# Kernel optimization log

Measured on AMD Instinct MI355X. Metric: run time of the kernel, lower is better.

## Reference

```python
import jax, jax.numpy as jnp
import numpy as np

DIM = 768
HEADS = 12
HEAD_DIM = DIM // HEADS


def setup_inputs() -> dict:
    key = jax.random.key(0)
    ks = jax.random.split(key, 5)
    B, N = 2, 2048
    x = jax.random.normal(ks[0], (B, N, DIM), dtype=jnp.float32)
    s = 1.0 / np.sqrt(DIM)
    qkv_w = jax.random.normal(ks[1], (3 * DIM, DIM), dtype=jnp.float32) * s
    qkv_b = jnp.zeros((3 * DIM,), dtype=jnp.float32)
    proj_w = jax.random.normal(ks[2], (DIM, DIM), dtype=jnp.float32) * s
    proj_b = jnp.zeros((DIM,), dtype=jnp.float32)
    return {"x": x, "qkv_w": qkv_w, "qkv_b": qkv_b, "proj_w": proj_w, "proj_b": proj_b}


def reference(x, qkv_w, qkv_b, proj_w, proj_b):
    B, N, C = x.shape
    scale = HEAD_DIM ** -0.5
    qkv = x @ qkv_w.T + qkv_b                      # [B,N,3C]
    qkv = qkv.reshape(B, N, 3, HEADS, HEAD_DIM)
    q = qkv[:, :, 0].transpose(0, 2, 1, 3)         # [B,H,N,D]
    k = qkv[:, :, 1].transpose(0, 2, 1, 3)
    v = qkv[:, :, 2].transpose(0, 2, 1, 3)
    attn = jnp.einsum('bhnd,bhmd->bhnm', q, k) * scale
    attn = jax.nn.softmax(attn, axis=-1)
    out = jnp.einsum('bhnm,bhmd->bhnd', attn, v)   # [B,H,N,D]
    out = out.transpose(0, 2, 1, 3).reshape(B, N, C)
    return out @ proj_w.T + proj_b
```

## Files before the change

kernel.cpp:

```cpp
#include <hip/hip_runtime.h>
#include <hip/hip_bf16.h>

typedef __bf16 bf16x8 __attribute__((ext_vector_type(8)));
typedef float f32x4 __attribute__((ext_vector_type(4)));
typedef float f32x16 __attribute__((ext_vector_type(16)));

#define SEQ   2048
#define NHEAD 12
#define NBH   24
#define QSCALE 0.18033688011112042f

#define CP16(g, l) __builtin_amdgcn_global_load_lds( \
    (const __attribute__((address_space(1))) unsigned int*)(g), \
    (__attribute__((address_space(3))) unsigned int*)(l), 16, 0, 0)

#define SUPER 1040
__device__ __forceinline__ int ldsoffK(int R, int c) {
  return (R >> 3) * SUPER + (R & 7) * 128 + ((c ^ (R & 7)) << 4);
}

__device__ __forceinline__ unsigned short f2bf(float f) {
  unsigned int u = __builtin_bit_cast(unsigned int, f);
  u += 0x7FFFu + ((u >> 16) & 1u);
  return (unsigned short)(u >> 16);
}
__device__ __forceinline__ unsigned int packbf2_trunc(float lo, float hi) {
  return __builtin_amdgcn_perm(__builtin_bit_cast(unsigned int, hi),
                               __builtin_bit_cast(unsigned int, lo), 0x07060302u);
}

#define NX4  786432
#define NW14 442368
__global__ __launch_bounds__(256) void cvt3_kernel(const float4* __restrict__ x,
                                                   const float4* __restrict__ w1,
                                                   const float4* __restrict__ w2,
                                                   ushort4* __restrict__ xo,
                                                   ushort4* __restrict__ w1o,
                                                   ushort4* __restrict__ w2o) {
  int i = blockIdx.x * 256 + threadIdx.x;
  const float4* s;
  ushort4* d;
  int j = i;
  if (i < NX4)               { s = x;  d = xo; }
  else if (i < NX4 + NW14)   { s = w1; d = w1o; j = i - NX4; }
  else                       { s = w2; d = w2o; j = i - (NX4 + NW14); }
  float4 v = s[j];
  ushort4 r;
  r.x = f2bf(v.x); r.y = f2bf(v.y); r.z = f2bf(v.z); r.w = f2bf(v.w);
  d[j] = r;
}

template <int BM, int BN, int MODE>
__global__ __launch_bounds__(256) void gemm_kernel(const unsigned short* __restrict__ X,
                                                   const unsigned short* __restrict__ W,
                                                   const float* __restrict__ bias,
                                                   unsigned short* __restrict__ Qb,
                                                   unsigned short* __restrict__ Kb,
                                                   unsigned short* __restrict__ Vtb,
                                                   float* __restrict__ Out) {
  constexpr int K = 768, BK = 64;
  constexpr int WM = BM / 2, WN = BN / 2;
  constexpr int MT = WM / 16, NT = WN / 16;
  __shared__ __align__(16) char Xs[(BM / 8) * SUPER];
  __shared__ __align__(16) char Ws[(BN / 8) * SUPER];

  const int tid = threadIdx.x;
  const int w = tid >> 6, lane = tid & 63, quad = lane >> 4, m16 = lane & 15;
  const int wm = w & 1, wn = w >> 1;
  const int row0 = blockIdx.y * BM, col0 = blockIdx.x * BN;

  f32x4 acc[MT][NT];
#pragma unroll
  for (int mt = 0; mt < MT; ++mt)
#pragma unroll
    for (int nt = 0; nt < NT; ++nt) acc[mt][nt] = (f32x4){0.f, 0.f, 0.f, 0.f};

  for (int k0 = 0; k0 < K; k0 += BK) {
    __syncthreads();
#pragma unroll
    for (int j = 0; j < BM / 32; ++j) {
      int e = tid + 256 * j, r = e >> 3, c8 = e & 7;
      CP16(X + (size_t)(row0 + r) * 768 + k0 + ((c8 ^ (r & 7)) << 3),
           Xs + (w + 4 * j) * SUPER + lane * 16);
    }
#pragma unroll
    for (int j = 0; j < BN / 32; ++j) {
      int e = tid + 256 * j, r = e >> 3, c8 = e & 7;
      CP16(W + (size_t)(col0 + r) * 768 + k0 + ((c8 ^ (r & 7)) << 3),
           Ws + (w + 4 * j) * SUPER + lane * 16);
    }
    __syncthreads();
#pragma unroll
    for (int ks = 0; ks < 2; ++ks) {
      bf16x8 a[MT], b[NT];
#pragma unroll
      for (int mt = 0; mt < MT; ++mt)
        a[mt] = *(const bf16x8*)(Xs + ldsoffK(wm * WM + mt * 16 + m16, quad + 4 * ks));
#pragma unroll
      for (int nt = 0; nt < NT; ++nt)
        b[nt] = *(const bf16x8*)(Ws + ldsoffK(wn * WN + nt * 16 + m16, quad + 4 * ks));
#pragma unroll
      for (int mt = 0; mt < MT; ++mt)
#pragma unroll
        for (int nt = 0; nt < NT; ++nt)
          acc[mt][nt] = __builtin_amdgcn_mfma_f32_16x16x32_bf16(a[mt], b[nt], acc[mt][nt], 0, 0, 0);
    }
  }

#pragma unroll
  for (int mt = 0; mt < MT; ++mt) {
#pragma unroll
    for (int nt = 0; nt < NT; ++nt) {
      const int m0 = row0 + wm * WM + mt * 16 + quad * 4;
      const int c = col0 + wn * WN + nt * 16 + m16;
      const float bia = bias[c];
      f32x4 v = acc[mt][nt];
      if constexpr (MODE == 0) {
        const int bidx = m0 >> 11, ns = m0 & 2047;
        if (c < 1536) {
          unsigned short* dst;
          float sc;
          int cc;
          if (c < 768) { cc = c; dst = Qb; sc = QSCALE; }
          else         { cc = c - 768; dst = Kb; sc = 1.0f; }
          const int h = cc >> 6, d = cc & 63;
          unsigned short* p = dst + ((size_t)(bidx * NHEAD + h) * SEQ + ns) * 64 + d;
          p[0]   = f2bf((v[0] + bia) * sc);
          p[64]  = f2bf((v[1] + bia) * sc);
          p[128] = f2bf((v[2] + bia) * sc);
          p[192] = f2bf((v[3] + bia) * sc);
        } else {
          const int cc = c - 1536, h = cc >> 6, d = cc & 63;
          const int ns2 = (ns & ~12) | ((ns & 4) << 1) | ((ns & 8) >> 1);
          ushort4 pk;
          pk.x = f2bf(v[0] + bia); pk.y = f2bf(v[1] + bia);
          pk.z = f2bf(v[2] + bia); pk.w = f2bf(v[3] + bia);
          *(ushort4*)(Vtb + ((size_t)(bidx * NHEAD + h) * 64 + d) * SEQ + ns2) = pk;
        }
      } else {
        float* o = Out + (size_t)m0 * 768 + c;
        o[0]       = v[0] + bia;
        o[768]     = v[1] + bia;
        o[2 * 768] = v[2] + bia;
        o[3 * 768] = v[3] + bia;
      }
    }
  }
}

__global__ __launch_bounds__(256, 3) void attn_kernel(const unsigned short* __restrict__ Qb,
                                                      const unsigned short* __restrict__ Kb,
                                                      const unsigned short* __restrict__ Vtb,
                                                      unsigned short* __restrict__ Ab) {
  __shared__ __align__(16) char KsB[2][2][4 * SUPER];
  __shared__ __align__(16) float Comb[2][2][4][64][4];
  __shared__ float Lc[2][64];

  const int tid = threadIdx.x;
  const int w = tid >> 6, lane = tid & 63, hi = lane >> 5, l32 = lane & 31;
  const int pair = w >> 1, qtile = w & 1;
  const int bh = blockIdx.x % NBH, qt = blockIdx.x / NBH;
  const int bb = bh / NHEAD, h = bh % NHEAD;
  const int q0 = qt * 64 + qtile * 32;

  const unsigned short* Qp = Qb + (size_t)bh * SEQ * 64;
  const unsigned short* Kph = Kb + (size_t)bh * SEQ * 64 + (size_t)pair * 1024 * 64;
  const unsigned short* vp0 = Vtb + (size_t)bh * 64 * SEQ + (size_t)l32 * SEQ + pair * 1024 + hi * 8;
  const unsigned short* vp1 = vp0 + (size_t)32 * SEQ;

  bf16x8 qf[4];
#pragma unroll
  for (int dc = 0; dc < 4; ++dc)
    qf[dc] = *(const bf16x8*)(Qp + (size_t)(q0 + l32) * 64 + dc * 16 + hi * 8);

  const unsigned short* srcK[2];
  int dK[2];
#pragma unroll
  for (int jj = 0; jj < 2; ++jj) {
    int e = qtile * 128 + jj * 64 + lane, r = e >> 3, c8 = e & 7;
    srcK[jj] = Kph + r * 64 + ((c8 ^ (r & 7)) << 3);
    dK[jj] = (qtile * 2 + jj) * SUPER + lane * 16;
  }
  int koff[4];
#pragma unroll
  for (int dc = 0; dc < 4; ++dc) koff[dc] = ldsoffK(l32, (dc << 1) | hi);

#pragma unroll
  for (int jj = 0; jj < 2; ++jj) CP16(srcK[jj], &KsB[pair][0][dK[jj]]);
  bf16x8 vfA[4], vfB[4];
  vfA[0] = *(const bf16x8*)(vp0);
  vfA[1] = *(const bf16x8*)(vp0 + 16);
  vfA[2] = *(const bf16x8*)(vp1);
  vfA[3] = *(const bf16x8*)(vp1 + 16);

  f32x16 o[2] = {};
  float l_i = 0.f;

#define ATTN_STEP(BUF, VC, VN, IT)                                                  \
  {                                                                                 \
    __syncthreads();                                                                \
    const char* kb = KsB[pair][BUF];                                                \
    bf16x8 kf[4];                                                                   \
    _Pragma("unroll") for (int dc = 0; dc < 4; ++dc)                                \
      kf[dc] = *(const bf16x8*)(kb + koff[dc]);                                     \
    if ((IT) < 31) {                                                                \
      _Pragma("unroll") for (int jj = 0; jj < 2; ++jj) {                            \
        srcK[jj] += 2048;                                                           \
        CP16(srcK[jj], &KsB[pair][1 - (BUF)][dK[jj]]);                              \
      }                                                                             \
      vp0 += 32; vp1 += 32;                                                         \
      VN[0] = *(const bf16x8*)(vp0);                                                \
      VN[1] = *(const bf16x8*)(vp0 + 16);                                           \
      VN[2] = *(const bf16x8*)(vp1);                                                \
      VN[3] = *(const bf16x8*)(vp1 + 16);                                           \
    }                                                                               \
    f32x16 s = {};                                                                  \
    _Pragma("unroll") for (int dc = 0; dc < 4; ++dc)                                \
      s = __builtin_amdgcn_mfma_f32_32x32x16_bf16(kf[dc], qf[dc], s, 0, 0, 0);      \
    float pv[16];                                                                   \
    _Pragma("unroll") for (int e = 0; e < 16; ++e)                                  \
      pv[e] = __builtin_amdgcn_exp2f(s[e]);                                         \
    float t0 = (pv[0] + pv[1]) + (pv[2] + pv[3]);                                   \
    float t1 = (pv[4] + pv[5]) + (pv[6] + pv[7]);                                   \
    float t2 = (pv[8] + pv[9]) + (pv[10] + pv[11]);                                 \
    float t3 = (pv[12] + pv[13]) + (pv[14] + pv[15]);                               \
    l_i += (t0 + t1) + (t2 + t3);                                                   \
    unsigned int pf[8];                                                             \
    _Pragma("unroll") for (int e2 = 0; e2 < 8; ++e2)                                \
      pf[e2] = packbf2_trunc(pv[2 * e2], pv[2 * e2 + 1]);                           \
    _Pragma("unroll") for (int kc2 = 0; kc2 < 2; ++kc2) {                           \
      bf16x8 pfrag = __builtin_bit_cast(bf16x8,                                     \
          make_uint4(pf[kc2 * 4], pf[kc2 * 4 + 1], pf[kc2 * 4 + 2], pf[kc2 * 4 + 3])); \
      o[0] = __builtin_amdgcn_mfma_f32_32x32x16_bf16(VC[kc2], pfrag, o[0], 0, 0, 0);     \
      o[1] = __builtin_amdgcn_mfma_f32_32x32x16_bf16(VC[2 + kc2], pfrag, o[1], 0, 0, 0); \
    }                                                                               \
  }

  for (int it2 = 0; it2 < 32; it2 += 2) {
    ATTN_STEP(0, vfA, vfB, it2);
    ATTN_STEP(1, vfB, vfA, it2 + 1);
  }
#undef ATTN_STEP

  l_i += __shfl_xor(l_i, 32);
  __syncthreads();
  if (pair == 1) {
#pragma unroll
    for (int dt = 0; dt < 2; ++dt)
#pragma unroll
      for (int run = 0; run < 4; ++run) {
        f32x4 v = {o[dt][run * 4], o[dt][run * 4 + 1], o[dt][run * 4 + 2], o[dt][run * 4 + 3]};
        *(f32x4*)&Comb[qtile][dt][run][lane][0] = v;
      }
    Lc[qtile][lane] = l_i;
  }
  __syncthreads();
  if (pair == 0) {
    l_i += Lc[qtile][lane];
    const float rl = __builtin_amdgcn_rcpf(l_i);
    unsigned short* base = Ab + ((size_t)bb * SEQ + q0 + l32) * 768 + h * 64;
#pragma unroll
    for (int dt = 0; dt < 2; ++dt) {
#pragma unroll
      for (int run = 0; run < 4; ++run) {
        f32x4 c = *(const f32x4*)&Comb[qtile][dt][run][lane][0];
        ushort4 pk;
        pk.x = f2bf((o[dt][run * 4 + 0] + c[0]) * rl);
        pk.y = f2bf((o[dt][run * 4 + 1] + c[1]) * rl);
        pk.z = f2bf((o[dt][run * 4 + 2] + c[2]) * rl);
        pk.w = f2bf((o[dt][run * 4 + 3] + c[3]) * rl);
        *(ushort4*)(base + dt * 32 + run * 8 + hi * 4) = pk;
      }
    }
  }
}

extern "C" void kernel_launch(void* const* d_in, const int* in_sizes, int n_in,
                              void* d_out, int out_size, void* d_ws, size_t ws_size,
                              hipStream_t stream) {
  const float* x      = (const float*)d_in[0];
  const float* qkv_w  = (const float*)d_in[1];
  const float* qkv_b  = (const float*)d_in[2];
  const float* proj_w = (const float*)d_in[3];
  const float* proj_b = (const float*)d_in[4];
  float* out = (float*)d_out;

  unsigned short* xb  = (unsigned short*)d_ws;
  unsigned short* wqb = xb + 3145728;
  unsigned short* wpb = wqb + 1769472;
  unsigned short* Qb  = wpb + 589824;
  unsigned short* Kb  = Qb + 3145728;
  unsigned short* Vtb = Kb + 3145728;
  unsigned short* Ab  = Vtb + 3145728;

  cvt3_kernel<<<5376, 256, 0, stream>>>((const float4*)x, (const float4*)qkv_w, (const float4*)proj_w,
                                        (ushort4*)xb, (ushort4*)wqb, (ushort4*)wpb);
  gemm_kernel<128, 96, 0><<<dim3(24, 32), 256, 0, stream>>>(xb, wqb, qkv_b, Qb, Kb, Vtb, nullptr);
  attn_kernel<<<768, 256, 0, stream>>>(Qb, Kb, Vtb, Ab);
  gemm_kernel<64, 96, 1><<<dim3(8, 64), 256, 0, stream>>>(Ab, wpb, proj_b, nullptr, nullptr, nullptr, out);
}
```

Before: 175.3 us.

## Split attention KV range four ways per block with one 32-row query tile

Each attention block now handles a single 32-row query tile, and each of its four waves processes a quarter of the key/value sequence instead of two waves per half. The grid doubles to 1536 blocks and launch bounds ask for 4 blocks per CU, which gives more parallelism and shorter per-wave loops. Each wave keeps its own double-buffered K tile in shared memory, reused afterwards for a three-way partial-sum combine. The cost is that Q fragments are loaded per wave with no sharing across query tiles, K loads into LDS are no longer shared across two query tiles, and the final reduction gets larger.

```diff
diff --git a/kernel.cpp b/kernel.cpp
--- a/kernel.cpp
+++ b/kernel.cpp
@@ -148,24 +148,23 @@
   }
 }
 
-__global__ __launch_bounds__(256, 3) void attn_kernel(const unsigned short* __restrict__ Qb,
+#define WKB   (2 * 4 * SUPER)
+#define COMBB (3 * 2 * 4 * 64 * 16)
+__global__ __launch_bounds__(256, 4) void attn_kernel(const unsigned short* __restrict__ Qb,
                                                       const unsigned short* __restrict__ Kb,
                                                       const unsigned short* __restrict__ Vtb,
                                                       unsigned short* __restrict__ Ab) {
-  __shared__ __align__(16) char KsB[2][2][4 * SUPER];
-  __shared__ __align__(16) float Comb[2][2][4][64][4];
-  __shared__ float Lc[2][64];
+  __shared__ __align__(16) char Smem[4 * WKB];
 
   const int tid = threadIdx.x;
   const int w = tid >> 6, lane = tid & 63, hi = lane >> 5, l32 = lane & 31;
-  const int pair = w >> 1, qtile = w & 1;
   const int bh = blockIdx.x % NBH, qt = blockIdx.x / NBH;
   const int bb = bh / NHEAD, h = bh % NHEAD;
-  const int q0 = qt * 64 + qtile * 32;
+  const int q0 = qt * 32;
 
   const unsigned short* Qp = Qb + (size_t)bh * SEQ * 64;
-  const unsigned short* Kph = Kb + (size_t)bh * SEQ * 64 + (size_t)pair * 1024 * 64;
-  const unsigned short* vp0 = Vtb + (size_t)bh * 64 * SEQ + (size_t)l32 * SEQ + pair * 1024 + hi * 8;
+  const unsigned short* Kph = Kb + (size_t)bh * SEQ * 64 + (size_t)w * 512 * 64;
+  const unsigned short* vp0 = Vtb + (size_t)bh * 64 * SEQ + (size_t)l32 * SEQ + w * 512 + hi * 8;
   const unsigned short* vp1 = vp0 + (size_t)32 * SEQ;
 
   bf16x8 qf[4];
@@ -173,20 +172,19 @@
   for (int dc = 0; dc < 4; ++dc)
     qf[dc] = *(const bf16x8*)(Qp + (size_t)(q0 + l32) * 64 + dc * 16 + hi * 8);
 
-  const unsigned short* srcK[2];
-  int dK[2];
-#pragma unroll
-  for (int jj = 0; jj < 2; ++jj) {
-    int e = qtile * 128 + jj * 64 + lane, r = e >> 3, c8 = e & 7;
+  char* const myK = Smem + w * WKB;
+  const unsigned short* srcK[4];
+#pragma unroll
+  for (int jj = 0; jj < 4; ++jj) {
+    int e = jj * 64 + lane, r = e >> 3, c8 = e & 7;
     srcK[jj] = Kph + r * 64 + ((c8 ^ (r & 7)) << 3);
-    dK[jj] = (qtile * 2 + jj) * SUPER + lane * 16;
   }
   int koff[4];
 #pragma unroll
   for (int dc = 0; dc < 4; ++dc) koff[dc] = ldsoffK(l32, (dc << 1) | hi);
 
 #pragma unroll
-  for (int jj = 0; jj < 2; ++jj) CP16(srcK[jj], &KsB[pair][0][dK[jj]]);
+  for (int jj = 0; jj < 4; ++jj) CP16(srcK[jj], myK + jj * SUPER + lane * 16);
   bf16x8 vfA[4], vfB[4];
   vfA[0] = *(const bf16x8*)(vp0);
   vfA[1] = *(const bf16x8*)(vp0 + 16);
@@ -199,14 +197,14 @@
 #define ATTN_STEP(BUF, VC, VN, IT)                                                  \
   {                                                                                 \
     __syncthreads();                                                                \
-    const char* kb = KsB[pair][BUF];                                                \
+    const char* kb = myK + (BUF) * (4 * SUPER);                                     \
     bf16x8 kf[4];                                                                   \
     _Pragma("unroll") for (int dc = 0; dc < 4; ++dc)                                \
       kf[dc] = *(const bf16x8*)(kb + koff[dc]);                                     \
-    if ((IT) < 31) {                                                                \
-      _Pragma("unroll") for (int jj = 0; jj < 2; ++jj) {                            \
+    if ((IT) < 15) {                                                                \
+      _Pragma("unroll") for (int jj = 0; jj < 4; ++jj) {                            \
         srcK[jj] += 2048;                                                           \
-        CP16(srcK[jj], &KsB[pair][1 - (BUF)][dK[jj]]);                              \
+        CP16(srcK[jj], myK + (1 - (BUF)) * (4 * SUPER) + jj * SUPER + lane * 16);   \
       }                                                                             \
       vp0 += 32; vp1 += 32;                                                         \
       VN[0] = *(const bf16x8*)(vp0);                                                \
@@ -236,39 +234,44 @@
     }                                                                               \
   }
 
-  for (int it2 = 0; it2 < 32; it2 += 2) {
+  for (int it2 = 0; it2 < 16; it2 += 2) {
     ATTN_STEP(0, vfA, vfB, it2);
     ATTN_STEP(1, vfB, vfA, it2 + 1);
   }
 #undef ATTN_STEP
 
   l_i += __shfl_xor(l_i, 32);
+  float* Comb = (float*)Smem;
+  float* Lc = (float*)(Smem + COMBB);
   __syncthreads();
-  if (pair == 1) {
+  if (w != 0) {
+    const int sp = w - 1;
 #pragma unroll
     for (int dt = 0; dt < 2; ++dt)
 #pragma unroll
       for (int run = 0; run < 4; ++run) {
         f32x4 v = {o[dt][run * 4], o[dt][run * 4 + 1], o[dt][run * 4 + 2], o[dt][run * 4 + 3]};
-        *(f32x4*)&Comb[qtile][dt][run][lane][0] = v;
+        *(f32x4*)&Comb[(((sp * 2 + dt) * 4 + run) * 64 + lane) * 4] = v;
       }
-    Lc[qtile][lane] = l_i;
+    Lc[sp * 64 + lane] = l_i;
   }
   __syncthreads();
-  if (pair == 0) {
-    l_i += Lc[qtile][lane];
+  if (w == 0) {
+    l_i += Lc[lane] + Lc[64 + lane] + Lc[128 + lane];
     const float rl = __builtin_amdgcn_rcpf(l_i);
     unsigned short* base = Ab + ((size_t)bb * SEQ + q0 + l32) * 768 + h * 64;
 #pragma unroll
     for (int dt = 0; dt < 2; ++dt) {
 #pragma unroll
       for (int run = 0; run < 4; ++run) {
-        f32x4 c = *(const f32x4*)&Comb[qtile][dt][run][lane][0];
+        f32x4 c0 = *(const f32x4*)&Comb[(((0 * 2 + dt) * 4 + run) * 64 + lane) * 4];
+        f32x4 c1 = *(const f32x4*)&Comb[(((1 * 2 + dt) * 4 + run) * 64 + lane) * 4];
+        f32x4 c2 = *(const f32x4*)&Comb[(((2 * 2 + dt) * 4 + run) * 64 + lane) * 4];
         ushort4 pk;
-        pk.x = f2bf((o[dt][run * 4 + 0] + c[0]) * rl);
-        pk.y = f2bf((o[dt][run * 4 + 1] + c[1]) * rl);
-        pk.z = f2bf((o[dt][run * 4 + 2] + c[2]) * rl);
-        pk.w = f2bf((o[dt][run * 4 + 3] + c[3]) * rl);
+        pk.x = f2bf((o[dt][run * 4 + 0] + c0[0] + c1[0] + c2[0]) * rl);
+        pk.y = f2bf((o[dt][run * 4 + 1] + c0[1] + c1[1] + c2[1]) * rl);
+        pk.z = f2bf((o[dt][run * 4 + 2] + c0[2] + c1[2] + c2[2]) * rl);
+        pk.w = f2bf((o[dt][run * 4 + 3] + c0[3] + c1[3] + c2[3]) * rl);
         *(ushort4*)(base + dt * 32 + run * 8 + hi * 4) = pk;
       }
     }
@@ -296,6 +299,6 @@
   cvt3_kernel<<<5376, 256, 0, stream>>>((const float4*)x, (const float4*)qkv_w, (const float4*)proj_w,
                                         (ushort4*)xb, (ushort4*)wqb, (ushort4*)wpb);
   gemm_kernel<128, 96, 0><<<dim3(24, 32), 256, 0, stream>>>(xb, wqb, qkv_b, Qb, Kb, Vtb, nullptr);
-  attn_kernel<<<768, 256, 0, stream>>>(Qb, Kb, Vtb, Ab);
+  attn_kernel<<<1536, 256, 0, stream>>>(Qb, Kb, Vtb, Ab);
   gemm_kernel<64, 96, 1><<<dim3(8, 64), 256, 0, stream>>>(Ab, wpb, proj_b, nullptr, nullptr, nullptr, out);
 }
```

New measurement: 217.0 us. +23.7%, slower.
